# Optimization experiments

Measured on AMD Instinct MI355X. Metric: run time of the kernel, lower is better.

## Reference

```python
import jax, jax.numpy as jnp
import numpy as np

B, S, D = 8, 1024, 512


def setup_inputs() -> dict:
    key = jax.random.key(0)
    k1, k2, k3, k4, k5, k6, k7 = jax.random.split(key, 7)
    inp = jax.random.normal(k1, (B, S, D), dtype=jnp.float32)
    aspect = jax.random.normal(k2, (B, S, D), dtype=jnp.float32)
    # lengths in [S//2, S], with max exactly S (the module requires max(len)==S)
    inp_len = jax.random.randint(k3, (B,), S // 2, S + 1).astype(jnp.float32)
    inp_len = inp_len.at[0].set(float(S))
    lim = float(np.sqrt(6.0 / (D + D)))  # xavier_uniform bound
    w1 = jax.random.uniform(k4, (D, D), jnp.float32, -lim, lim)
    b1 = jax.random.uniform(k5, (D,), jnp.float32, -lim, lim)
    w2 = jax.random.uniform(k6, (D, D), jnp.float32, -lim, lim)
    b2 = jax.random.uniform(k7, (D,), jnp.float32, -lim, lim)
    return {"inp": inp, "inp_len": inp_len, "aspect": aspect,
            "w1": w1, "b1": b1, "w2": w2, "b2": b2}


def reference(inp, inp_len, aspect, w1, b1, w2, b2):
    # inp, aspect: [B,S,D]; inp_len: [B] float lengths with max == S
    Bv, Sv, Dv = inp.shape
    scale = jnp.sqrt(inp_len)[:, None, None]                      # [B,1,1]
    att = jnp.einsum('bsd,btd->bst', aspect, inp) / scale          # [B,S,S]
    # mask over the query (row) dimension, as in the original expand
    mask = (jnp.arange(Sv)[None, :] < inp_len.astype(jnp.int32)[:, None]).astype(inp.dtype)  # [B,S]
    exp = att * mask[:, :, None]
    att_n = exp / (jnp.sum(exp, axis=-1, keepdims=True) + 1e-4)    # linear (non-exp) normalize
    weighted = jnp.einsum('bst,btd->bsd', att_n, inp)              # [B,S,D]
    ffn_inp = weighted + (inp + aspect) * mask[:, :, None]
    # FFN: two square linears with relu, plus inner residual
    o1 = jax.nn.relu(jnp.einsum('bsd,ed->bse', ffn_inp, w1) + b1)
    o2 = jax.nn.relu(jnp.einsum('bsd,ed->bse', o1, w2) + b2)
    ffn_out = o2 + ffn_inp
    final = ffn_inp + ffn_out
    return final / jnp.linalg.norm(final, axis=2, keepdims=True)
```

## Files before the change

kernel.cpp:

```cpp
#include <hip/hip_runtime.h>

#define Bq 8
#define Sq 1024
#define Dq 512

typedef __attribute__((ext_vector_type(8))) short bf16x8;
typedef __attribute__((ext_vector_type(4))) float f32x4;

__device__ __forceinline__ unsigned short f2bf(float f) {
  unsigned int u = __float_as_uint(f);
  return (unsigned short)((u + 0x7fffu + ((u >> 16) & 1u)) >> 16);
}

__device__ __forceinline__ void load_lds16(const unsigned short* g, unsigned short* l) {
  __builtin_amdgcn_global_load_lds(
      (const __attribute__((address_space(1))) unsigned int*)g,
      (__attribute__((address_space(3))) unsigned int*)l, 16, 0, 0);
}


__global__ __launch_bounds__(256) void prep_all(
    const float* __restrict__ inp, const float* __restrict__ aspect,
    const float* __restrict__ w1, const float* __restrict__ w2,
    unsigned short* __restrict__ inpT, float* __restrict__ partial,
    unsigned short* __restrict__ asp_bf,
    unsigned short* __restrict__ w1b, unsigned short* __restrict__ w2b) {
  __shared__ unsigned short tile[32][33];
  __shared__ float csum[8][33];
  int idx = blockIdx.x;
  int tid = threadIdx.x;
  if (idx < 4096) {
    int b = idx & 7;
    int tt = (idx >> 3) & 31;
    int t0 = tt * 32, d0 = (idx >> 8) * 32;
    int tx = tid & 31, ty = tid >> 5;
    const float* src = inp + ((size_t)b * Sq + t0) * Dq + d0;
    float part = 0.f;
#pragma unroll
    for (int i = 0; i < 4; ++i) {
      float v = src[(size_t)(ty + i * 8) * Dq + tx];
      tile[ty + i * 8][tx] = f2bf(v);
      part += v;
    }
    csum[ty][tx] = part;
    __syncthreads();
    unsigned short* dst = inpT + (size_t)b * Dq * Sq;
#pragma unroll
    for (int i = 0; i < 4; ++i)
      dst[(size_t)(d0 + ty + i * 8) * Sq + t0 + tx] = tile[tx][ty + i * 8];
    if (ty == 0) {
      float s = 0.f;
#pragma unroll
      for (int i = 0; i < 8; ++i) s += csum[i][tx];
      partial[((size_t)b * 32 + tt) * Dq + d0 + tx] = s;
    }
  } else if (idx < 4608) {
    int blk = idx - 4096;
    const float* s = aspect + (size_t)blk * 8192 + tid * 4;
    unsigned short* d = asp_bf + (size_t)blk * 8192 + tid * 4;
#pragma unroll
    for (int j = 0; j < 8; ++j) {
      float4 v = *(const float4*)(s + j * 1024);
      ushort4 o; o.x = f2bf(v.x); o.y = f2bf(v.y); o.z = f2bf(v.z); o.w = f2bf(v.w);
      *(ushort4*)(d + j * 1024) = o;
    }
  } else {
    int blk = idx - 4608;
    const float* src = (blk < 256) ? w1 : w2;
    unsigned short* dst = (blk < 256) ? w1b : w2b;
    int li = ((blk & 255) * 256 + tid) * 4;
    int n = li >> 9, k = li & 511;
    float4 v = *(const float4*)(src + li);
    ushort4 o; o.x = f2bf(v.x); o.y = f2bf(v.y); o.z = f2bf(v.z); o.w = f2bf(v.w);
    int off = (k >> 5) * 16384 + ((n << 2) + ((k & 31) >> 3)) * 8 + (k & 7);
    *(ushort4*)(dst + off) = o;
  }
}

__global__ __launch_bounds__(256, 5) void gram_fac(
    const unsigned short* __restrict__ inpT, const float* __restrict__ partial,
    const float* __restrict__ aspect, const float* __restrict__ lenv,
    unsigned short* __restrict__ Gm, float* __restrict__ fac) {
  __shared__ unsigned short sA[2][32 * 64];
  __shared__ unsigned short sB[2][64 * 64];
  int idx = blockIdx.x;
  int tid = threadIdx.x;
  int lane = tid & 63, wave = tid >> 6;

  if (idx >= 1024) {
    float* cs = (float*)sA;
    int fblk = idx - 1024;
    int b = fblk >> 6;
    int s0 = (fblk & 63) * 16;
#pragma unroll
    for (int h = 0; h < 2; ++h) {
      int d = h * 256 + tid;
      float s = 0.f;
      const float* p = partial + (size_t)b * 32 * Dq + d;
#pragma unroll
      for (int t = 0; t < 32; ++t) s += p[t * Dq];
      cs[d] = s;
    }
    __syncthreads();
    int g = lane >> 4, lr = lane & 15;
    int row = s0 + wave * 4 + g;
    const float* a = aspect + ((size_t)b * Sq + row) * Dq + lr * 32;
    float sum = 0.f;
#pragma unroll
    for (int j = 0; j < 8; ++j) {
      float4 v = *(const float4*)(a + j * 4);
      const float* c = cs + lr * 32 + j * 4;
      sum += v.x * c[0] + v.y * c[1] + v.z * c[2] + v.w * c[3];
    }
#pragma unroll
    for (int off = 1; off < 16; off <<= 1) sum += __shfl_xor(sum, off, 64);
    if (lr == 0) {
      float len = lenv[b];
      float scale = sqrtf(len);
      float f = 0.f;
      if (row < (int)len) f = 1.f / (scale * (sum / scale + 1e-4f));
      fac[b * Sq + row] = f;
    }
    return;
  }

  const int K = 1024;
  int b = idx & 7;
  int tile = idx >> 3;
  int bm = tile & 15, bn = tile >> 4;
  const unsigned short* Ab = inpT + (size_t)b * Dq * Sq + (size_t)bm * 32 * K;
  const unsigned short* Bb = inpT + (size_t)b * Dq * Sq + (size_t)bn * 64 * K;
  int lr = lane & 15, lq = lane >> 4;
  int x7 = lr & 7;
  int l3 = lane >> 3, l7 = lane & 7;

  const unsigned short* gA = Ab + (size_t)(wave * 8 + l3) * K + (l7 ^ l3) * 8;
  const unsigned short* gB = Bb + (size_t)(wave * 16 + l3) * K + (l7 ^ l3) * 8;
  int dbaseA = (wave * 64 + lane) * 8;
  int dbaseB0 = (wave * 128 + lane) * 8;
  int dbaseB1 = (wave * 128 + 64 + lane) * 8;

  f32x4 acc[2] = {};

  auto issue = [&](int buf, int k0) {
    load_lds16(gA + k0, &sA[buf][dbaseA]);
    load_lds16(gB + k0, &sB[buf][dbaseB0]);
    load_lds16(gB + (size_t)8 * K + k0, &sB[buf][dbaseB1]);
  };

  int wm = (wave & 1) * 16, wn = (wave >> 1) * 32;
  issue(0, 0);
#pragma unroll
  for (int it = 0; it < 16; ++it) {
    int cur = it & 1;
    if (it + 1 < 16) {
      issue(cur ^ 1, (it + 1) << 6);
      asm volatile("s_waitcnt vmcnt(3)" ::: "memory");
    } else {
      asm volatile("s_waitcnt vmcnt(0)" ::: "memory");
    }
    __builtin_amdgcn_s_barrier();
#pragma unroll
    for (int c = 0; c < 2; ++c) {
      int g = c * 4 + lq;
      bf16x8 a0 = *(const bf16x8*)&sA[cur][((wm + lr) * 8 + (g ^ x7)) * 8];
      bf16x8 b0 = *(const bf16x8*)&sB[cur][((wn + lr) * 8 + (g ^ x7)) * 8];
      bf16x8 b1 = *(const bf16x8*)&sB[cur][((wn + 16 + lr) * 8 + (g ^ x7)) * 8];
      acc[0] = __builtin_amdgcn_mfma_f32_16x16x32_bf16(a0, b0, acc[0], 0, 0, 0);
      acc[1] = __builtin_amdgcn_mfma_f32_16x16x32_bf16(a0, b1, acc[1], 0, 0, 0);
    }
    asm volatile("s_waitcnt lgkmcnt(0)" ::: "memory");
    __builtin_amdgcn_sched_barrier(0);
    __builtin_amdgcn_s_barrier();
  }

  unsigned short* sP = sA[0];
#pragma unroll
  for (int ni = 0; ni < 2; ++ni)
#pragma unroll
    for (int i = 0; i < 4; ++i) {
      int rl = wm + lq * 4 + i;
      int ccl = wn + ni * 16 + lr;
      sP[ccl * 32 + rl] = f2bf(acc[ni][i]);
    }
  __syncthreads();
  unsigned short* Ob = Gm + (size_t)b * 512 * 512 + (size_t)bm * 16384 + (size_t)bn * 2048;
  *(bf16x8*)(Ob + tid * 8) = *(const bf16x8*)(sP + tid * 8);
}

#define LP 520
#define MEGA_SMEM (32 * LP * 2 + 3 * 32768 + 512)

__global__ __launch_bounds__(512, 2) void mega_ffn(
    const unsigned short* __restrict__ aspb, const unsigned short* __restrict__ G,
    const unsigned short* __restrict__ w1b, const unsigned short* __restrict__ w2b,
    const float* __restrict__ b1, const float* __restrict__ b2,
    const float* __restrict__ inp, const float* __restrict__ aspect,
    const float* __restrict__ fac, const float* __restrict__ lenv,
    float* __restrict__ out) {
  extern __shared__ char smem[];
  unsigned short* ldsA = (unsigned short*)smem;
  unsigned short* wbuf = (unsigned short*)(smem + 32 * LP * 2);
  float* ssqW = (float*)(smem + 32 * LP * 2 + 3 * 32768);
  int tid = threadIdx.x;
  int lane = tid & 63, wave = tid >> 6;
  int mg = wave >> 2, ng = wave & 3;
  int lr = lane & 15, lq = lane >> 4;
  int bid = ((blockIdx.x & 7) << 5) | (blockIdx.x >> 3);
  int r0 = bid * 32;
  int b = r0 >> 10;
  int c0 = ng * 128;
  int arow = r0 + mg * 16 + lr;

  bf16x8 af[16];
  f32x4 acc[8];
  f32x4 ffnv[8];

  int soff = (wave * 64 + lane) * 8;
  auto stage = [&](int buf, int kc, const unsigned short* Bsrc) {
    const unsigned short* src = Bsrc + kc * 16384;
    unsigned short* dstb = wbuf + buf * 16384;
#pragma unroll
    for (int i = 0; i < 4; ++i)
      load_lds16(src + i * 4096 + soff, dstb + i * 4096 + soff);
  };

  auto gemmPhase = [&](const unsigned short* Bsrc) {
#pragma unroll
    for (int t = 0; t < 8; ++t) acc[t] = (f32x4){0.f, 0.f, 0.f, 0.f};
    stage(0, 0, Bsrc);
    stage(1, 1, Bsrc);
#pragma unroll
    for (int kc = 0; kc < 16; ++kc) {
      int cur = kc % 3;
      if (kc < 14) {
        stage((kc + 2) % 3, kc + 2, Bsrc);
        asm volatile("s_waitcnt vmcnt(8)" ::: "memory");
      } else if (kc == 14) {
        asm volatile("s_waitcnt vmcnt(4)" ::: "memory");
      } else {
        asm volatile("s_waitcnt vmcnt(0)" ::: "memory");
      }
      __builtin_amdgcn_s_barrier();
      bf16x8 bfr[8];
#pragma unroll
      for (int t = 0; t < 8; ++t)
        bfr[t] = *(const bf16x8*)&wbuf[cur * 16384 + (size_t)((c0 + t * 16 + lr) * 4 + lq) * 8];
#pragma unroll
      for (int t = 0; t < 8; ++t)
        acc[t] = __builtin_amdgcn_mfma_f32_16x16x32_bf16(af[kc], bfr[t], acc[t], 0, 0, 0);
      asm volatile("s_waitcnt lgkmcnt(0)" ::: "memory");
      __builtin_amdgcn_sched_barrier(0);
      __builtin_amdgcn_s_barrier();
    }
  };

#pragma unroll
  for (int j = 0; j < 16; ++j)
    af[j] = *(const bf16x8*)(aspb + (size_t)arow * 512 + j * 32 + lq * 8);
  gemmPhase(G + (size_t)b * 512 * 512);
  int len = (int)lenv[b];
  float facv[4];
#pragma unroll
  for (int i = 0; i < 4; ++i) facv[i] = fac[r0 + mg * 16 + lq * 4 + i];
#pragma unroll
  for (int t = 0; t < 8; ++t) {
#pragma unroll
    for (int i = 0; i < 4; ++i) {
      int r = r0 + mg * 16 + lq * 4 + i;
      size_t idx = (size_t)r * 512 + c0 + t * 16 + lr;
      float add = ((r & 1023) < len) ? (inp[idx] + aspect[idx]) : 0.f;
      float v = acc[t][i] * facv[i] + add;
      ffnv[t][i] = v;
      ldsA[(mg * 16 + lq * 4 + i) * LP + c0 + t * 16 + lr] = f2bf(v);
    }
  }
  __syncthreads();

#pragma unroll
  for (int j = 0; j < 16; ++j)
    af[j] = *(const bf16x8*)&ldsA[(mg * 16 + lr) * LP + j * 32 + lq * 8];
  __syncthreads();
  gemmPhase(w1b);
  float biasv[8];
#pragma unroll
  for (int t = 0; t < 8; ++t) biasv[t] = b1[c0 + t * 16 + lr];
#pragma unroll
  for (int t = 0; t < 8; ++t)
#pragma unroll
    for (int i = 0; i < 4; ++i)
      ldsA[(mg * 16 + lq * 4 + i) * LP + c0 + t * 16 + lr] =
          f2bf(fmaxf(acc[t][i] + biasv[t], 0.f));
  __syncthreads();

#pragma unroll
  for (int j = 0; j < 16; ++j)
    af[j] = *(const bf16x8*)&ldsA[(mg * 16 + lr) * LP + j * 32 + lq * 8];
  __syncthreads();
  gemmPhase(w2b);
#pragma unroll
  for (int t = 0; t < 8; ++t) biasv[t] = b2[c0 + t * 16 + lr];
  float ssq[4] = {0.f, 0.f, 0.f, 0.f};
#pragma unroll
  for (int t = 0; t < 8; ++t)
#pragma unroll
    for (int i = 0; i < 4; ++i) {
      float v = 2.f * ffnv[t][i] + fmaxf(acc[t][i] + biasv[t], 0.f);
      ffnv[t][i] = v;
      ssq[i] += v * v;
    }
#pragma unroll
  for (int off = 1; off < 16; off <<= 1)
#pragma unroll
    for (int i = 0; i < 4; ++i) ssq[i] += __shfl_xor(ssq[i], off, 64);
  if (lr == 0)
#pragma unroll
    for (int i = 0; i < 4; ++i) ssqW[(mg * 4 + ng) * 16 + lq * 4 + i] = ssq[i];
  __syncthreads();
  float rn[4];
#pragma unroll
  for (int i = 0; i < 4; ++i) {
    float s = ssqW[(mg * 4 + 0) * 16 + lq * 4 + i] + ssqW[(mg * 4 + 1) * 16 + lq * 4 + i] +
              ssqW[(mg * 4 + 2) * 16 + lq * 4 + i] + ssqW[(mg * 4 + 3) * 16 + lq * 4 + i];
    rn[i] = 1.f / sqrtf(s);
  }
#pragma unroll
  for (int t = 0; t < 8; ++t)
#pragma unroll
    for (int i = 0; i < 4; ++i) {
      int r = r0 + mg * 16 + lq * 4 + i;
      out[(size_t)r * 512 + c0 + t * 16 + lr] = ffnv[t][i] * rn[i];
    }
}

extern "C" void kernel_launch(void* const* d_in, const int* in_sizes, int n_in,
                              void* d_out, int out_size, void* d_ws, size_t ws_size,
                              hipStream_t stream) {
  const float* inp = (const float*)d_in[0];
  const float* inp_len = (const float*)d_in[1];
  const float* aspect = (const float*)d_in[2];
  const float* w1 = (const float*)d_in[3];
  const float* b1 = (const float*)d_in[4];
  const float* w2 = (const float*)d_in[5];
  const float* b2 = (const float*)d_in[6];
  float* out = (float*)d_out;

  char* W = (char*)d_ws;
  const size_t MB = 1ull << 20;
  unsigned short* asp_bf = (unsigned short*)(W + 0);
  unsigned short* inpT   = (unsigned short*)(W + 8 * MB);
  unsigned short* Gm     = (unsigned short*)(W + 16 * MB);
  unsigned short* w1bf   = (unsigned short*)(W + 20 * MB);
  unsigned short* w2bf   = (unsigned short*)(W + 20 * MB + 512 * 1024);
  float*          partial= (float*)(W + 21 * MB);
  float*          fac    = (float*)(W + 22 * MB);

  prep_all<<<5120, 256, 0, stream>>>(inp, aspect, w1, w2,
                                     inpT, partial, asp_bf, w1bf, w2bf);

  gram_fac<<<1536, 256, 0, stream>>>(inpT, partial, aspect, inp_len, Gm, fac);

  hipFuncSetAttribute((const void*)mega_ffn,
                      hipFuncAttributeMaxDynamicSharedMemorySize, MEGA_SMEM);
  mega_ffn<<<256, 512, MEGA_SMEM, stream>>>(
      asp_bf, Gm, w1bf, w2bf, b1, b2, inp, aspect, fac, inp_len, out);
}
```

Before: 144.5 us.

## Remap mega_ffn waves to 32x64 tiles and XOR-swizzle weight/G LDS layout

Each of the 8 waves in mega_ffn now covers all 32 rows and a 64-column slice, instead of a 16x128 tile. Each weight fragment loaded from LDS now feeds two MFMAs, which halves B-operand LDS reads per wave, though each wave holds twice as many A fragments in registers. The packed weight layout written by prep_all and the G tile written by gram_fac use an XOR swizzle on the 8-element groups, so B-fragment reads from LDS avoid bank conflicts. The per-wave sum-of-squares buffer grows to hold 8 partials per row.

```diff
diff --git a/kernel.cpp b/kernel.cpp
--- a/kernel.cpp
+++ b/kernel.cpp
@@ -72,7 +72,8 @@
     int n = li >> 9, k = li & 511;
     float4 v = *(const float4*)(src + li);
     ushort4 o; o.x = f2bf(v.x); o.y = f2bf(v.y); o.z = f2bf(v.z); o.w = f2bf(v.w);
-    int off = (k >> 5) * 16384 + ((n << 2) + ((k & 31) >> 3)) * 8 + (k & 7);
+    int x = ((k >> 3) & 3) ^ ((n >> 1) & 3);
+    int off = (k >> 5) * 16384 + n * 32 + x * 8 + (k & 7);
     *(ushort4*)(dst + off) = o;
   }
 }
@@ -181,7 +182,8 @@
     for (int i = 0; i < 4; ++i) {
       int rl = wm + lq * 4 + i;
       int ccl = wn + ni * 16 + lr;
-      sP[ccl * 32 + rl] = f2bf(acc[ni][i]);
+      int x = (rl >> 3) ^ ((ccl >> 1) & 3);
+      sP[ccl * 32 + x * 8 + (rl & 7)] = f2bf(acc[ni][i]);
     }
   __syncthreads();
   unsigned short* Ob = Gm + (size_t)b * 512 * 512 + (size_t)bm * 16384 + (size_t)bn * 2048;
@@ -189,7 +191,7 @@
 }
 
 #define LP 520
-#define MEGA_SMEM (32 * LP * 2 + 3 * 32768 + 512)
+#define MEGA_SMEM (32 * LP * 2 + 3 * 32768 + 1024)
 
 __global__ __launch_bounds__(512, 2) void mega_ffn(
     const unsigned short* __restrict__ aspb, const unsigned short* __restrict__ G,
@@ -204,19 +206,20 @@
   float* ssqW = (float*)(smem + 32 * LP * 2 + 3 * 32768);
   int tid = threadIdx.x;
   int lane = tid & 63, wave = tid >> 6;
-  int mg = wave >> 2, ng = wave & 3;
   int lr = lane & 15, lq = lane >> 4;
   int bid = ((blockIdx.x & 7) << 5) | (blockIdx.x >> 3);
   int r0 = bid * 32;
   int b = r0 >> 10;
-  int c0 = ng * 128;
-  int arow = r0 + mg * 16 + lr;
-
-  bf16x8 af[16];
-  f32x4 acc[8];
-  f32x4 ffnv[8];
-
-  int soff = (wave * 64 + lane) * 8;
+  int c0 = wave * 64;
+
+  bf16x8 af2[2][16];
+  f32x4 acc[2][4];
+  float ffnv[2][4][4];
+
+  int bx = (lq ^ ((lr >> 1) & 3)) * 8;
+  int rdbase = (c0 + lr) * 32 + bx;
+
+  int soff = tid * 8;
   auto stage = [&](int buf, int kc, const unsigned short* Bsrc) {
     const unsigned short* src = Bsrc + kc * 16384;
     unsigned short* dstb = wbuf + buf * 16384;
@@ -227,7 +230,9 @@
 
   auto gemmPhase = [&](const unsigned short* Bsrc) {
 #pragma unroll
-    for (int t = 0; t < 8; ++t) acc[t] = (f32x4){0.f, 0.f, 0.f, 0.f};
+    for (int m = 0; m < 2; ++m)
+#pragma unroll
+      for (int t = 0; t < 4; ++t) acc[m][t] = (f32x4){0.f, 0.f, 0.f, 0.f};
     stage(0, 0, Bsrc);
     stage(1, 1, Bsrc);
 #pragma unroll
@@ -242,13 +247,15 @@
         asm volatile("s_waitcnt vmcnt(0)" ::: "memory");
       }
       __builtin_amdgcn_s_barrier();
-      bf16x8 bfr[8];
-#pragma unroll
-      for (int t = 0; t < 8; ++t)
-        bfr[t] = *(const bf16x8*)&wbuf[cur * 16384 + (size_t)((c0 + t * 16 + lr) * 4 + lq) * 8];
-#pragma unroll
-      for (int t = 0; t < 8; ++t)
-        acc[t] = __builtin_amdgcn_mfma_f32_16x16x32_bf16(af[kc], bfr[t], acc[t], 0, 0, 0);
+      bf16x8 bfr[4];
+#pragma unroll
+      for (int t = 0; t < 4; ++t)
+        bfr[t] = *(const bf16x8*)&wbuf[cur * 16384 + rdbase + t * 512];
+#pragma unroll
+      for (int t = 0; t < 4; ++t) {
+        acc[0][t] = __builtin_amdgcn_mfma_f32_16x16x32_bf16(af2[0][kc], bfr[t], acc[0][t], 0, 0, 0);
+        acc[1][t] = __builtin_amdgcn_mfma_f32_16x16x32_bf16(af2[1][kc], bfr[t], acc[1][t], 0, 0, 0);
+      }
       asm volatile("s_waitcnt lgkmcnt(0)" ::: "memory");
       __builtin_amdgcn_sched_barrier(0);
       __builtin_amdgcn_s_barrier();
@@ -256,81 +263,105 @@
   };
 
 #pragma unroll
-  for (int j = 0; j < 16; ++j)
-    af[j] = *(const bf16x8*)(aspb + (size_t)arow * 512 + j * 32 + lq * 8);
+  for (int m = 0; m < 2; ++m)
+#pragma unroll
+    for (int j = 0; j < 16; ++j)
+      af2[m][j] = *(const bf16x8*)(aspb + (size_t)(r0 + m * 16 + lr) * 512 + j * 32 + lq * 8);
   gemmPhase(G + (size_t)b * 512 * 512);
   int len = (int)lenv[b];
-  float facv[4];
-#pragma unroll
-  for (int i = 0; i < 4; ++i) facv[i] = fac[r0 + mg * 16 + lq * 4 + i];
-#pragma unroll
-  for (int t = 0; t < 8; ++t) {
+  float facv[2][4];
+#pragma unroll
+  for (int m = 0; m < 2; ++m)
+#pragma unroll
+    for (int i = 0; i < 4; ++i) facv[m][i] = fac[r0 + m * 16 + lq * 4 + i];
+#pragma unroll
+  for (int m = 0; m < 2; ++m)
+#pragma unroll
+    for (int t = 0; t < 4; ++t)
+#pragma unroll
+      for (int i = 0; i < 4; ++i) {
+        int rr = m * 16 + lq * 4 + i;
+        int r = r0 + rr;
+        size_t idx = (size_t)r * 512 + c0 + t * 16 + lr;
+        float add = ((r & 1023) < len) ? (inp[idx] + aspect[idx]) : 0.f;
+        float v = acc[m][t][i] * facv[m][i] + add;
+        ffnv[m][t][i] = v;
+        ldsA[rr * LP + c0 + t * 16 + lr] = f2bf(v);
+      }
+  __syncthreads();
+
+#pragma unroll
+  for (int m = 0; m < 2; ++m)
+#pragma unroll
+    for (int j = 0; j < 16; ++j)
+      af2[m][j] = *(const bf16x8*)&ldsA[(m * 16 + lr) * LP + j * 32 + lq * 8];
+  __syncthreads();
+  gemmPhase(w1b);
+  float biasv[4];
+#pragma unroll
+  for (int t = 0; t < 4; ++t) biasv[t] = b1[c0 + t * 16 + lr];
+#pragma unroll
+  for (int m = 0; m < 2; ++m)
+#pragma unroll
+    for (int t = 0; t < 4; ++t)
+#pragma unroll
+      for (int i = 0; i < 4; ++i) {
+        int rr = m * 16 + lq * 4 + i;
+        ldsA[rr * LP + c0 + t * 16 + lr] = f2bf(fmaxf(acc[m][t][i] + biasv[t], 0.f));
+      }
+  __syncthreads();
+
+#pragma unroll
+  for (int m = 0; m < 2; ++m)
+#pragma unroll
+    for (int j = 0; j < 16; ++j)
+      af2[m][j] = *(const bf16x8*)&ldsA[(m * 16 + lr) * LP + j * 32 + lq * 8];
+  __syncthreads();
+  gemmPhase(w2b);
+#pragma unroll
+  for (int t = 0; t < 4; ++t) biasv[t] = b2[c0 + t * 16 + lr];
+  float ssq[2][4] = {{0.f, 0.f, 0.f, 0.f}, {0.f, 0.f, 0.f, 0.f}};
+#pragma unroll
+  for (int m = 0; m < 2; ++m)
+#pragma unroll
+    for (int t = 0; t < 4; ++t)
+#pragma unroll
+      for (int i = 0; i < 4; ++i) {
+        float v = 2.f * ffnv[m][t][i] + fmaxf(acc[m][t][i] + biasv[t], 0.f);
+        ffnv[m][t][i] = v;
+        ssq[m][i] += v * v;
+      }
+#pragma unroll
+  for (int off = 1; off < 16; off <<= 1)
+#pragma unroll
+    for (int m = 0; m < 2; ++m)
+#pragma unroll
+      for (int i = 0; i < 4; ++i) ssq[m][i] += __shfl_xor(ssq[m][i], off, 64);
+  if (lr == 0)
+#pragma unroll
+    for (int m = 0; m < 2; ++m)
+#pragma unroll
+      for (int i = 0; i < 4; ++i) ssqW[wave * 32 + m * 16 + lq * 4 + i] = ssq[m][i];
+  __syncthreads();
+  float rn[2][4];
+#pragma unroll
+  for (int m = 0; m < 2; ++m)
 #pragma unroll
     for (int i = 0; i < 4; ++i) {
-      int r = r0 + mg * 16 + lq * 4 + i;
-      size_t idx = (size_t)r * 512 + c0 + t * 16 + lr;
-      float add = ((r & 1023) < len) ? (inp[idx] + aspect[idx]) : 0.f;
-      float v = acc[t][i] * facv[i] + add;
-      ffnv[t][i] = v;
-      ldsA[(mg * 16 + lq * 4 + i) * LP + c0 + t * 16 + lr] = f2bf(v);
-    }
-  }
-  __syncthreads();
-
-#pragma unroll
-  for (int j = 0; j < 16; ++j)
-    af[j] = *(const bf16x8*)&ldsA[(mg * 16 + lr) * LP + j * 32 + lq * 8];
-  __syncthreads();
-  gemmPhase(w1b);
-  float biasv[8];
-#pragma unroll
-  for (int t = 0; t < 8; ++t) biasv[t] = b1[c0 + t * 16 + lr];
-#pragma unroll
-  for (int t = 0; t < 8; ++t)
-#pragma unroll
-    for (int i = 0; i < 4; ++i)
-      ldsA[(mg * 16 + lq * 4 + i) * LP + c0 + t * 16 + lr] =
-          f2bf(fmaxf(acc[t][i] + biasv[t], 0.f));
-  __syncthreads();
-
-#pragma unroll
-  for (int j = 0; j < 16; ++j)
-    af[j] = *(const bf16x8*)&ldsA[(mg * 16 + lr) * LP + j * 32 + lq * 8];
-  __syncthreads();
-  gemmPhase(w2b);
-#pragma unroll
-  for (int t = 0; t < 8; ++t) biasv[t] = b2[c0 + t * 16 + lr];
-  float ssq[4] = {0.f, 0.f, 0.f, 0.f};
-#pragma unroll
-  for (int t = 0; t < 8; ++t)
-#pragma unroll
-    for (int i = 0; i < 4; ++i) {
-      float v = 2.f * ffnv[t][i] + fmaxf(acc[t][i] + biasv[t], 0.f);
-      ffnv[t][i] = v;
-      ssq[i] += v * v;
-    }
-#pragma unroll
-  for (int off = 1; off < 16; off <<= 1)
-#pragma unroll
-    for (int i = 0; i < 4; ++i) ssq[i] += __shfl_xor(ssq[i], off, 64);
-  if (lr == 0)
-#pragma unroll
-    for (int i = 0; i < 4; ++i) ssqW[(mg * 4 + ng) * 16 + lq * 4 + i] = ssq[i];
-  __syncthreads();
-  float rn[4];
-#pragma unroll
-  for (int i = 0; i < 4; ++i) {
-    float s = ssqW[(mg * 4 + 0) * 16 + lq * 4 + i] + ssqW[(mg * 4 + 1) * 16 + lq * 4 + i] +
-              ssqW[(mg * 4 + 2) * 16 + lq * 4 + i] + ssqW[(mg * 4 + 3) * 16 + lq * 4 + i];
-    rn[i] = 1.f / sqrtf(s);
-  }
-#pragma unroll
-  for (int t = 0; t < 8; ++t)
-#pragma unroll
-    for (int i = 0; i < 4; ++i) {
-      int r = r0 + mg * 16 + lq * 4 + i;
-      out[(size_t)r * 512 + c0 + t * 16 + lr] = ffnv[t][i] * rn[i];
-    }
+      float s = 0.f;
+#pragma unroll
+      for (int w = 0; w < 8; ++w) s += ssqW[w * 32 + m * 16 + lq * 4 + i];
+      rn[m][i] = 1.f / sqrtf(s);
+    }
+#pragma unroll
+  for (int m = 0; m < 2; ++m)
+#pragma unroll
+    for (int t = 0; t < 4; ++t)
+#pragma unroll
+      for (int i = 0; i < 4; ++i) {
+        int r = r0 + m * 16 + lq * 4 + i;
+        out[(size_t)r * 512 + c0 + t * 16 + lr] = ffnv[m][t][i] * rn[m][i];
+      }
 }
 
 extern "C" void kernel_launch(void* const* d_in, const int* in_sizes, int n_in,
```

After: 143.9 us. Within noise of the previous version (-0.4%).

## Retile FFN to 16-row blocks, swizzle LDS, and regroup prep work across kernels

Applied to the files above, without the earlier changes.

The fused FFN kernel now processes 16 rows per block with 8 waves each owning 64 columns, doubling the grid to 512 blocks and allowing 4 blocks per CU via smaller LDS and a double-buffered (instead of triple) weight pipeline. Padded LDS rows are replaced by XOR swizzles for the activation tile, the weight layout, and the Gram output layout to avoid bank conflicts. The transpose prep uses 64x64 tiles with vectorized accesses, and the aspect/weight bf16 conversions move into the gram kernel's grid so they overlap with Gram computation. Trade-offs include shallower prefetch and less B-fragment reuse per block.

```diff
diff --git a/kernel.cpp b/kernel.cpp
--- a/kernel.cpp
+++ b/kernel.cpp
@@ -19,74 +19,81 @@
 }
 
 
-__global__ __launch_bounds__(256) void prep_all(
-    const float* __restrict__ inp, const float* __restrict__ aspect,
+__global__ __launch_bounds__(256) void prep_t(
+    const float* __restrict__ inp,
+    unsigned short* __restrict__ inpT, float* __restrict__ partial) {
+  __shared__ unsigned short tile[64][66];
+  __shared__ float csum[16][64];
+  int idx = blockIdx.x;
+  int tid = threadIdx.x;
+  int b = idx & 7, tt = (idx >> 3) & 15, dd = idx >> 7;
+  int r = tid >> 4, c4 = (tid & 15) * 4;
+  const float* src = inp + ((size_t)b * Sq + tt * 64) * Dq + dd * 64;
+  float cp0 = 0.f, cp1 = 0.f, cp2 = 0.f, cp3 = 0.f;
+#pragma unroll
+  for (int p = 0; p < 4; ++p) {
+    float4 v = *(const float4*)(src + (size_t)(r + p * 16) * Dq + c4);
+    ushort4 o; o.x = f2bf(v.x); o.y = f2bf(v.y); o.z = f2bf(v.z); o.w = f2bf(v.w);
+    *(ushort4*)&tile[r + p * 16][c4] = o;
+    cp0 += v.x; cp1 += v.y; cp2 += v.z; cp3 += v.w;
+  }
+  csum[r][c4] = cp0; csum[r][c4 + 1] = cp1; csum[r][c4 + 2] = cp2; csum[r][c4 + 3] = cp3;
+  __syncthreads();
+  unsigned short* dst = inpT + (size_t)b * Dq * Sq + (size_t)dd * 64 * Sq + tt * 64;
+#pragma unroll
+  for (int p = 0; p < 4; ++p) {
+    int d = (tid >> 4) + p * 16;
+    int tq = (tid & 15) * 4;
+    ushort4 o;
+    o.x = tile[tq][d]; o.y = tile[tq + 1][d]; o.z = tile[tq + 2][d]; o.w = tile[tq + 3][d];
+    *(ushort4*)(dst + (size_t)d * Sq + tq) = o;
+  }
+  if (tid < 64) {
+    float s = 0.f;
+#pragma unroll
+    for (int rr = 0; rr < 16; ++rr) s += csum[rr][tid];
+    partial[((size_t)b * 16 + tt) * Dq + dd * 64 + tid] = s;
+  }
+}
+
+__global__ __launch_bounds__(256, 5) void gram_fac(
+    const unsigned short* __restrict__ inpT, const float* __restrict__ partial,
+    const float* __restrict__ aspect, const float* __restrict__ lenv,
     const float* __restrict__ w1, const float* __restrict__ w2,
-    unsigned short* __restrict__ inpT, float* __restrict__ partial,
+    unsigned short* __restrict__ Gm, float* __restrict__ fac,
     unsigned short* __restrict__ asp_bf,
     unsigned short* __restrict__ w1b, unsigned short* __restrict__ w2b) {
-  __shared__ unsigned short tile[32][33];
-  __shared__ float csum[8][33];
+  __shared__ unsigned short sA[2][32 * 64];
+  __shared__ unsigned short sB[2][64 * 64];
   int idx = blockIdx.x;
   int tid = threadIdx.x;
-  if (idx < 4096) {
-    int b = idx & 7;
-    int tt = (idx >> 3) & 31;
-    int t0 = tt * 32, d0 = (idx >> 8) * 32;
-    int tx = tid & 31, ty = tid >> 5;
-    const float* src = inp + ((size_t)b * Sq + t0) * Dq + d0;
-    float part = 0.f;
-#pragma unroll
-    for (int i = 0; i < 4; ++i) {
-      float v = src[(size_t)(ty + i * 8) * Dq + tx];
-      tile[ty + i * 8][tx] = f2bf(v);
-      part += v;
-    }
-    csum[ty][tx] = part;
-    __syncthreads();
-    unsigned short* dst = inpT + (size_t)b * Dq * Sq;
-#pragma unroll
-    for (int i = 0; i < 4; ++i)
-      dst[(size_t)(d0 + ty + i * 8) * Sq + t0 + tx] = tile[tx][ty + i * 8];
-    if (ty == 0) {
-      float s = 0.f;
-#pragma unroll
-      for (int i = 0; i < 8; ++i) s += csum[i][tx];
-      partial[((size_t)b * 32 + tt) * Dq + d0 + tx] = s;
-    }
-  } else if (idx < 4608) {
-    int blk = idx - 4096;
-    const float* s = aspect + (size_t)blk * 8192 + tid * 4;
-    unsigned short* d = asp_bf + (size_t)blk * 8192 + tid * 4;
-#pragma unroll
-    for (int j = 0; j < 8; ++j) {
-      float4 v = *(const float4*)(s + j * 1024);
-      ushort4 o; o.x = f2bf(v.x); o.y = f2bf(v.y); o.z = f2bf(v.z); o.w = f2bf(v.w);
-      *(ushort4*)(d + j * 1024) = o;
-    }
-  } else {
-    int blk = idx - 4608;
+  int lane = tid & 63, wave = tid >> 6;
+
+  if (idx >= 2048) {
+    int blk = idx - 2048;
     const float* src = (blk < 256) ? w1 : w2;
     unsigned short* dst = (blk < 256) ? w1b : w2b;
     int li = ((blk & 255) * 256 + tid) * 4;
     int n = li >> 9, k = li & 511;
     float4 v = *(const float4*)(src + li);
     ushort4 o; o.x = f2bf(v.x); o.y = f2bf(v.y); o.z = f2bf(v.z); o.w = f2bf(v.w);
-    int off = (k >> 5) * 16384 + ((n << 2) + ((k & 31) >> 3)) * 8 + (k & 7);
+    int x = ((k >> 3) & 3) ^ ((n >> 1) & 3);
+    int off = (k >> 5) * 16384 + n * 32 + x * 8 + (k & 7);
     *(ushort4*)(dst + off) = o;
-  }
-}
-
-__global__ __launch_bounds__(256, 5) void gram_fac(
-    const unsigned short* __restrict__ inpT, const float* __restrict__ partial,
-    const float* __restrict__ aspect, const float* __restrict__ lenv,
-    unsigned short* __restrict__ Gm, float* __restrict__ fac) {
-  __shared__ unsigned short sA[2][32 * 64];
-  __shared__ unsigned short sB[2][64 * 64];
-  int idx = blockIdx.x;
-  int tid = threadIdx.x;
-  int lane = tid & 63, wave = tid >> 6;
-
+    return;
+  }
+  if (idx >= 1536) {
+    int blk = idx - 1536;
+    const float* s = aspect + (size_t)blk * 8192 + tid * 4;
+    unsigned short* d = asp_bf + (size_t)blk * 8192 + tid * 4;
+#pragma unroll
+    for (int j = 0; j < 8; ++j) {
+      float4 v = *(const float4*)(s + j * 1024);
+      ushort4 o; o.x = f2bf(v.x); o.y = f2bf(v.y); o.z = f2bf(v.z); o.w = f2bf(v.w);
+      *(ushort4*)(d + j * 1024) = o;
+    }
+    return;
+  }
   if (idx >= 1024) {
     float* cs = (float*)sA;
     int fblk = idx - 1024;
@@ -96,9 +103,9 @@
     for (int h = 0; h < 2; ++h) {
       int d = h * 256 + tid;
       float s = 0.f;
-      const float* p = partial + (size_t)b * 32 * Dq + d;
-#pragma unroll
-      for (int t = 0; t < 32; ++t) s += p[t * Dq];
+      const float* p = partial + (size_t)b * 16 * Dq + d;
+#pragma unroll
+      for (int t = 0; t < 16; ++t) s += p[t * Dq];
       cs[d] = s;
     }
     __syncthreads();
@@ -181,17 +188,17 @@
     for (int i = 0; i < 4; ++i) {
       int rl = wm + lq * 4 + i;
       int ccl = wn + ni * 16 + lr;
-      sP[ccl * 32 + rl] = f2bf(acc[ni][i]);
+      int x = (rl >> 3) ^ ((ccl >> 1) & 3);
+      sP[ccl * 32 + x * 8 + (rl & 7)] = f2bf(acc[ni][i]);
     }
   __syncthreads();
   unsigned short* Ob = Gm + (size_t)b * 512 * 512 + (size_t)bm * 16384 + (size_t)bn * 2048;
   *(bf16x8*)(Ob + tid * 8) = *(const bf16x8*)(sP + tid * 8);
 }
 
-#define LP 520
-#define MEGA_SMEM (32 * LP * 2 + 3 * 32768 + 512)
-
-__global__ __launch_bounds__(512, 2) void mega_ffn(
+#define MEGA_SMEM (16 * 512 * 2 + 2 * 16384 * 2)
+
+__global__ __launch_bounds__(512, 4) void mega_ffn(
     const unsigned short* __restrict__ aspb, const unsigned short* __restrict__ G,
     const unsigned short* __restrict__ w1b, const unsigned short* __restrict__ w2b,
     const float* __restrict__ b1, const float* __restrict__ b2,
@@ -200,23 +207,29 @@
     float* __restrict__ out) {
   extern __shared__ char smem[];
   unsigned short* ldsA = (unsigned short*)smem;
-  unsigned short* wbuf = (unsigned short*)(smem + 32 * LP * 2);
-  float* ssqW = (float*)(smem + 32 * LP * 2 + 3 * 32768);
+  unsigned short* wbuf = (unsigned short*)(smem + 16 * 512 * 2);
   int tid = threadIdx.x;
   int lane = tid & 63, wave = tid >> 6;
-  int mg = wave >> 2, ng = wave & 3;
   int lr = lane & 15, lq = lane >> 4;
-  int bid = ((blockIdx.x & 7) << 5) | (blockIdx.x >> 3);
-  int r0 = bid * 32;
-  int b = r0 >> 10;
-  int c0 = ng * 128;
-  int arow = r0 + mg * 16 + lr;
+  int xb = blockIdx.x;
+  int bid = ((xb & 7) << 6) | (xb >> 3);
+  int r0 = bid * 16;
+  int b = bid >> 6;
+  int c0 = wave * 64;
 
   bf16x8 af[16];
-  f32x4 acc[8];
-  f32x4 ffnv[8];
-
-  int soff = (wave * 64 + lane) * 8;
+  f32x4 acc[4];
+  float ffnv[4][4];
+
+  int bx = (lq ^ ((lr >> 1) & 3)) * 8;
+  int rdbase = (c0 + lr) * 32 + bx;
+
+  auto aoff = [&](int rr, int c) {
+    int cq = c >> 3;
+    return rr * 512 + ((cq ^ (rr & 7)) << 3) + (c & 7);
+  };
+
+  int soff = tid * 8;
   auto stage = [&](int buf, int kc, const unsigned short* Bsrc) {
     const unsigned short* src = Bsrc + kc * 16384;
     unsigned short* dstb = wbuf + buf * 16384;
@@ -227,27 +240,24 @@
 
   auto gemmPhase = [&](const unsigned short* Bsrc) {
 #pragma unroll
-    for (int t = 0; t < 8; ++t) acc[t] = (f32x4){0.f, 0.f, 0.f, 0.f};
+    for (int t = 0; t < 4; ++t) acc[t] = (f32x4){0.f, 0.f, 0.f, 0.f};
     stage(0, 0, Bsrc);
-    stage(1, 1, Bsrc);
 #pragma unroll
     for (int kc = 0; kc < 16; ++kc) {
-      int cur = kc % 3;
-      if (kc < 14) {
-        stage((kc + 2) % 3, kc + 2, Bsrc);
-        asm volatile("s_waitcnt vmcnt(8)" ::: "memory");
-      } else if (kc == 14) {
+      int cur = kc & 1;
+      if (kc < 15) {
+        stage(cur ^ 1, kc + 1, Bsrc);
         asm volatile("s_waitcnt vmcnt(4)" ::: "memory");
       } else {
         asm volatile("s_waitcnt vmcnt(0)" ::: "memory");
       }
       __builtin_amdgcn_s_barrier();
-      bf16x8 bfr[8];
-#pragma unroll
-      for (int t = 0; t < 8; ++t)
-        bfr[t] = *(const bf16x8*)&wbuf[cur * 16384 + (size_t)((c0 + t * 16 + lr) * 4 + lq) * 8];
-#pragma unroll
-      for (int t = 0; t < 8; ++t)
+      bf16x8 bfr[4];
+#pragma unroll
+      for (int t = 0; t < 4; ++t)
+        bfr[t] = *(const bf16x8*)&wbuf[cur * 16384 + rdbase + t * 512];
+#pragma unroll
+      for (int t = 0; t < 4; ++t)
         acc[t] = __builtin_amdgcn_mfma_f32_16x16x32_bf16(af[kc], bfr[t], acc[t], 0, 0, 0);
       asm volatile("s_waitcnt lgkmcnt(0)" ::: "memory");
       __builtin_amdgcn_sched_barrier(0);
@@ -257,52 +267,53 @@
 
 #pragma unroll
   for (int j = 0; j < 16; ++j)
-    af[j] = *(const bf16x8*)(aspb + (size_t)arow * 512 + j * 32 + lq * 8);
+    af[j] = *(const bf16x8*)(aspb + (size_t)(r0 + lr) * 512 + j * 32 + lq * 8);
   gemmPhase(G + (size_t)b * 512 * 512);
   int len = (int)lenv[b];
   float facv[4];
 #pragma unroll
-  for (int i = 0; i < 4; ++i) facv[i] = fac[r0 + mg * 16 + lq * 4 + i];
-#pragma unroll
-  for (int t = 0; t < 8; ++t) {
-#pragma unroll
-    for (int i = 0; i < 4; ++i) {
-      int r = r0 + mg * 16 + lq * 4 + i;
+  for (int i = 0; i < 4; ++i) facv[i] = fac[r0 + lq * 4 + i];
+#pragma unroll
+  for (int t = 0; t < 4; ++t)
+#pragma unroll
+    for (int i = 0; i < 4; ++i) {
+      int rr = lq * 4 + i;
+      int r = r0 + rr;
       size_t idx = (size_t)r * 512 + c0 + t * 16 + lr;
       float add = ((r & 1023) < len) ? (inp[idx] + aspect[idx]) : 0.f;
       float v = acc[t][i] * facv[i] + add;
       ffnv[t][i] = v;
-      ldsA[(mg * 16 + lq * 4 + i) * LP + c0 + t * 16 + lr] = f2bf(v);
-    }
-  }
+      ldsA[aoff(rr, c0 + t * 16 + lr)] = f2bf(v);
+    }
   __syncthreads();
 
 #pragma unroll
   for (int j = 0; j < 16; ++j)
-    af[j] = *(const bf16x8*)&ldsA[(mg * 16 + lr) * LP + j * 32 + lq * 8];
+    af[j] = *(const bf16x8*)&ldsA[aoff(lr, j * 32 + lq * 8)];
   __syncthreads();
   gemmPhase(w1b);
-  float biasv[8];
-#pragma unroll
-  for (int t = 0; t < 8; ++t) biasv[t] = b1[c0 + t * 16 + lr];
-#pragma unroll
-  for (int t = 0; t < 8; ++t)
-#pragma unroll
-    for (int i = 0; i < 4; ++i)
-      ldsA[(mg * 16 + lq * 4 + i) * LP + c0 + t * 16 + lr] =
-          f2bf(fmaxf(acc[t][i] + biasv[t], 0.f));
+  float biasv[4];
+#pragma unroll
+  for (int t = 0; t < 4; ++t) biasv[t] = b1[c0 + t * 16 + lr];
+#pragma unroll
+  for (int t = 0; t < 4; ++t)
+#pragma unroll
+    for (int i = 0; i < 4; ++i) {
+      int rr = lq * 4 + i;
+      ldsA[aoff(rr, c0 + t * 16 + lr)] = f2bf(fmaxf(acc[t][i] + biasv[t], 0.f));
+    }
   __syncthreads();
 
 #pragma unroll
   for (int j = 0; j < 16; ++j)
-    af[j] = *(const bf16x8*)&ldsA[(mg * 16 + lr) * LP + j * 32 + lq * 8];
+    af[j] = *(const bf16x8*)&ldsA[aoff(lr, j * 32 + lq * 8)];
   __syncthreads();
   gemmPhase(w2b);
 #pragma unroll
-  for (int t = 0; t < 8; ++t) biasv[t] = b2[c0 + t * 16 + lr];
+  for (int t = 0; t < 4; ++t) biasv[t] = b2[c0 + t * 16 + lr];
   float ssq[4] = {0.f, 0.f, 0.f, 0.f};
 #pragma unroll
-  for (int t = 0; t < 8; ++t)
+  for (int t = 0; t < 4; ++t)
 #pragma unroll
     for (int i = 0; i < 4; ++i) {
       float v = 2.f * ffnv[t][i] + fmaxf(acc[t][i] + biasv[t], 0.f);
@@ -313,22 +324,24 @@
   for (int off = 1; off < 16; off <<= 1)
 #pragma unroll
     for (int i = 0; i < 4; ++i) ssq[i] += __shfl_xor(ssq[i], off, 64);
+  float* ssqW = (float*)wbuf;
   if (lr == 0)
 #pragma unroll
-    for (int i = 0; i < 4; ++i) ssqW[(mg * 4 + ng) * 16 + lq * 4 + i] = ssq[i];
+    for (int i = 0; i < 4; ++i) ssqW[wave * 16 + lq * 4 + i] = ssq[i];
   __syncthreads();
   float rn[4];
 #pragma unroll
   for (int i = 0; i < 4; ++i) {
-    float s = ssqW[(mg * 4 + 0) * 16 + lq * 4 + i] + ssqW[(mg * 4 + 1) * 16 + lq * 4 + i] +
-              ssqW[(mg * 4 + 2) * 16 + lq * 4 + i] + ssqW[(mg * 4 + 3) * 16 + lq * 4 + i];
+    float s = 0.f;
+#pragma unroll
+    for (int w = 0; w < 8; ++w) s += ssqW[w * 16 + lq * 4 + i];
     rn[i] = 1.f / sqrtf(s);
   }
 #pragma unroll
-  for (int t = 0; t < 8; ++t)
-#pragma unroll
-    for (int i = 0; i < 4; ++i) {
-      int r = r0 + mg * 16 + lq * 4 + i;
+  for (int t = 0; t < 4; ++t)
+#pragma unroll
+    for (int i = 0; i < 4; ++i) {
+      int r = r0 + lq * 4 + i;
       out[(size_t)r * 512 + c0 + t * 16 + lr] = ffnv[t][i] * rn[i];
     }
 }
@@ -355,13 +368,13 @@
   float*          partial= (float*)(W + 21 * MB);
   float*          fac    = (float*)(W + 22 * MB);
 
-  prep_all<<<5120, 256, 0, stream>>>(inp, aspect, w1, w2,
-                                     inpT, partial, asp_bf, w1bf, w2bf);
-
-  gram_fac<<<1536, 256, 0, stream>>>(inpT, partial, aspect, inp_len, Gm, fac);
+  prep_t<<<1024, 256, 0, stream>>>(inp, inpT, partial);
+
+  gram_fac<<<2560, 256, 0, stream>>>(inpT, partial, aspect, inp_len, w1, w2,
+                                     Gm, fac, asp_bf, w1bf, w2bf);
 
   hipFuncSetAttribute((const void*)mega_ffn,
                       hipFuncAttributeMaxDynamicSharedMemorySize, MEGA_SMEM);
-  mega_ffn<<<256, 512, MEGA_SMEM, stream>>>(
+  mega_ffn<<<512, 512, MEGA_SMEM, stream>>>(
       asp_bf, Gm, w1bf, w2bf, b1, b2, inp, aspect, fac, inp_len, out);
 }
```

New measurement: 152.3 us. 1.05x slower.
